# Kernel tuning notes

Measured on AMD Instinct MI355X. Metric: run time of the kernel, lower is better.

Reference implementation:

```python
import jax, jax.numpy as jnp
import numpy as np

D_MODEL = 1024
N_HEADS = 16
D_K = D_MODEL // N_HEADS
B, S = 2, 2048


def setup_inputs() -> dict:
    key = jax.random.key(0)
    ks = jax.random.split(key, 12)
    s = 1.0 / np.sqrt(D_MODEL)
    inp = {
        "query": jax.random.normal(ks[0], (B, S, D_MODEL), jnp.float32),
        "key": jax.random.normal(ks[1], (B, S, D_MODEL), jnp.float32),
        "value": jax.random.normal(ks[2], (B, S, D_MODEL), jnp.float32),
        "W_q": jax.random.uniform(ks[3], (D_MODEL, D_MODEL), jnp.float32, -s, s),
        "b_q": jnp.zeros((D_MODEL,), jnp.float32),
        "W_k": jax.random.uniform(ks[4], (D_MODEL, D_MODEL), jnp.float32, -s, s),
        "b_k": jnp.zeros((D_MODEL,), jnp.float32),
        "W_v": jax.random.uniform(ks[5], (D_MODEL, D_MODEL), jnp.float32, -s, s),
        "b_v": jnp.zeros((D_MODEL,), jnp.float32),
        "W_o": jax.random.uniform(ks[6], (D_MODEL, D_MODEL), jnp.float32, -s, s),
        "b_o": jnp.zeros((D_MODEL,), jnp.float32),
        "ln_gamma": jnp.ones((D_MODEL,), jnp.float32),
        "ln_beta": jnp.zeros((D_MODEL,), jnp.float32),
    }
    return inp


def _layer_norm(x, gamma, beta, eps=1e-5):
    mu = jnp.mean(x, axis=-1, keepdims=True)
    var = jnp.var(x, axis=-1, keepdims=True)
    return (x - mu) * jax.lax.rsqrt(var + eps) * gamma + beta


def reference(query, key, value, W_q, b_q, W_k, b_k, W_v, b_v, W_o, b_o, ln_gamma, ln_beta):
    b, s, _ = query.shape
    # projections -> [b, h, s, d_k]
    q = (query @ W_q.T + b_q).reshape(b, s, N_HEADS, D_K).transpose(0, 2, 1, 3)
    k = (key @ W_k.T + b_k).reshape(b, s, N_HEADS, D_K).transpose(0, 2, 1, 3)
    v = (value @ W_v.T + b_v).reshape(b, s, N_HEADS, D_K).transpose(0, 2, 1, 3)
    # scaled dot-product attention (no mask)
    scores = jnp.einsum('bhqd,bhkd->bhqk', q, k) / jnp.sqrt(jnp.float32(D_K))
    attn = jax.nn.softmax(scores, axis=-1)
    ctx = jnp.einsum('bhqk,bhkd->bhqd', attn, v)  # [b,h,s,d_k]
    ctx = ctx.transpose(0, 2, 1, 3).reshape(b, s, D_MODEL)
    out = ctx @ W_o.T + b_o
    # residual uses the PROJECTED query (quirk of original module); dropout=identity (eval)
    resid = q.transpose(0, 2, 1, 3).reshape(b, s, D_MODEL)
    return _layer_norm(out + resid, ln_gamma, ln_beta)
```

## Files before the change

kernel.cpp:

```cpp
#include <hip/hip_runtime.h>

#define DM 1024
#define NH 16
#define DKq 64
#define BB 2
#define SS 2048
#define MTOT 4096

typedef __attribute__((ext_vector_type(4))) float f32x4;
typedef __attribute__((ext_vector_type(16))) float f32x16;
typedef __attribute__((ext_vector_type(8))) short s16x8;
typedef __attribute__((ext_vector_type(4))) short s16x4;
typedef __attribute__((ext_vector_type(4))) unsigned short u16x4;

__device__ __forceinline__ unsigned short f2bf(float f) {
    unsigned u = __float_as_uint(f);
    u += 0x7fff + ((u >> 16) & 1);
    return (unsigned short)(u >> 16);
}

__device__ __forceinline__ float bf2f(unsigned short x) {
    return __uint_as_float((unsigned)x << 16);
}

__device__ __forceinline__ s16x8 cvt8(f32x4 a, f32x4 b) {
    s16x8 r;
    r[0] = (short)f2bf(a[0]); r[1] = (short)f2bf(a[1]);
    r[2] = (short)f2bf(a[2]); r[3] = (short)f2bf(a[3]);
    r[4] = (short)f2bf(b[0]); r[5] = (short)f2bf(b[1]);
    r[6] = (short)f2bf(b[2]); r[7] = (short)f2bf(b[3]);
    return r;
}

__device__ __forceinline__ unsigned pktr(float a, float b) {
    return (__float_as_uint(a) >> 16) | (__float_as_uint(b) & 0xFFFF0000u);
}

__device__ __forceinline__ void gload_lds16(const void* g, void* l) {
    __builtin_amdgcn_global_load_lds(
        (const __attribute__((address_space(1))) unsigned int*)g,
        (__attribute__((address_space(3))) unsigned int*)l,
        16, 0, 0);
}

__global__ __launch_bounds__(256)
void cvt_kernel(const float* __restrict__ s0, const float* __restrict__ s1,
                const float* __restrict__ s2, const float* __restrict__ s3,
                const float* __restrict__ s4, const float* __restrict__ s5,
                const float* __restrict__ s6,
                unsigned short* __restrict__ Xb, unsigned short* __restrict__ Wb)
{
    const int seg = blockIdx.y;
    const float* src;
    unsigned short* dst;
    int n;
    if (seg < 3) {
        src = (seg == 0) ? s0 : (seg == 1) ? s1 : s2;
        dst = Xb + (size_t)seg * (MTOT * DM);
        n = MTOT * DM;
    } else {
        src = (seg == 3) ? s3 : (seg == 4) ? s4 : (seg == 5) ? s5 : s6;
        dst = Wb + (size_t)(seg - 3) * (DM * DM);
        n = DM * DM;
    }
    const int stride = gridDim.x * 256;
    for (int i = blockIdx.x * 256 + threadIdx.x; i * 8 < n; i += stride) {
        f32x4 a = *(const f32x4*)(src + (size_t)i * 8);
        f32x4 b = *(const f32x4*)(src + (size_t)i * 8 + 4);
        *(s16x8*)(dst + (size_t)i * 8) = cvt8(a, b);
    }
}

__global__ __launch_bounds__(256)
void proj_kernel(const unsigned short* __restrict__ Xb,
                 const unsigned short* __restrict__ Wb,
                 const float* __restrict__ bq, const float* __restrict__ bk,
                 const float* __restrict__ bv,
                 unsigned short* __restrict__ Qh, unsigned short* __restrict__ Kh,
                 unsigned short* __restrict__ Vt)
{
    const int z = blockIdx.z;
    const unsigned short* X = Xb + (size_t)z * (MTOT * DM);
    const unsigned short* W = Wb + (size_t)z * (DM * DM);
    const float* bias = (z == 0) ? bq : (z == 1) ? bk : bv;

    const int m0 = blockIdx.y * 128;
    const int n0 = blockIdx.x * 128;
    const int tid  = threadIdx.x;
    const int lane = tid & 63;
    const int w    = tid >> 6;
    const int wm   = w >> 1, wn = w & 1;

    __shared__ __align__(16) short lA[128 * 64];
    __shared__ __align__(16) short lB[128 * 64];

    f32x4 acc[4][4];
#pragma unroll
    for (int i = 0; i < 4; i++)
#pragma unroll
        for (int j = 0; j < 4; j++) acc[i][j] = (f32x4)(0.f);

    const int lrow = lane >> 3;
    const int lcg  = (lane & 7) ^ lrow;

    for (int kt = 0; kt < 16; ++kt) {
        const int k0 = kt * 64;
#pragma unroll
        for (int p = 0; p < 4; ++p) {
            int c = w * 4 + p;
            int row = c * 8 + lrow;
            gload_lds16(X + (size_t)(m0 + row) * DM + k0 + lcg * 8,
                        (char*)lA + c * 1024);
            gload_lds16(W + (size_t)(n0 + row) * DM + k0 + lcg * 8,
                        (char*)lB + c * 1024);
        }
        __syncthreads();
#pragma unroll
        for (int kk = 0; kk < 2; ++kk) {
            s16x8 af[4], bf[4];
#pragma unroll
            for (int i = 0; i < 4; i++) {
                int row = wm * 64 + i * 16 + (lane & 15);
                int byte = (kk * 64 + 16 * (lane >> 4)) ^ ((row & 7) << 4);
                af[i] = *(const s16x8*)((const char*)lA + row * 128 + byte);
            }
#pragma unroll
            for (int i = 0; i < 4; i++) {
                int row = wn * 64 + i * 16 + (lane & 15);
                int byte = (kk * 64 + 16 * (lane >> 4)) ^ ((row & 7) << 4);
                bf[i] = *(const s16x8*)((const char*)lB + row * 128 + byte);
            }
#pragma unroll
            for (int i = 0; i < 4; i++)
#pragma unroll
                for (int j = 0; j < 4; j++)
                    acc[i][j] = __builtin_amdgcn_mfma_f32_16x16x32_bf16(
                        af[i], bf[j], acc[i][j], 0, 0, 0);
        }
        __syncthreads();
    }

#pragma unroll
    for (int i = 0; i < 4; i++) {
#pragma unroll
        for (int j = 0; j < 4; j++) {
            int rg0 = m0 + wm * 64 + i * 16 + 4 * (lane >> 4);
            int cg  = n0 + wn * 64 + j * 16 + (lane & 15);
            int b = rg0 >> 11, s0 = rg0 & 2047, h = cg >> 6, d = cg & 63;
            float bv_ = bias[cg];
            if (z == 2) {
                u16x4 st;
#pragma unroll
                for (int e = 0; e < 4; e++) st[e] = f2bf(acc[i][j][e] + bv_);
                *(u16x4*)&Vt[(((size_t)(b * NH + h)) * DKq + d) * SS + s0] = st;
            } else {
                unsigned short* P = (z == 0) ? Qh : Kh;
#pragma unroll
                for (int e = 0; e < 4; e++)
                    P[(((size_t)(b * NH + h)) * SS + s0 + e) * DKq + d] =
                        f2bf(acc[i][j][e] + bv_);
            }
        }
    }
}

__device__ __forceinline__ void attn_tile32(
    const char* __restrict__ lkc, const char* __restrict__ lvc,
    const s16x8* aq, int l31, int hi,
    f32x16& o0, f32x16& o1, float& lrun)
{
    const float K2 = 0.18033688011112042f;
    const float FS = 4.0f * K2;

    f32x16 s0 = (f32x16)(0.f), s1 = (f32x16)(0.f);
    __builtin_amdgcn_s_setprio(1);
#pragma unroll
    for (int kkd = 0; kkd < 4; kkd++) {
        {
            int row = l31;
            int byte = (32 * kkd + 16 * hi) ^ ((row & 7) << 4);
            s16x8 ak = *(const s16x8*)(lkc + row * 128 + byte);
            s0 = __builtin_amdgcn_mfma_f32_32x32x16_bf16(ak, aq[kkd], s0, 0, 0, 0);
        }
        {
            int row = 32 + l31;
            int byte = (32 * kkd + 16 * hi) ^ ((row & 7) << 4);
            s16x8 ak = *(const s16x8*)(lkc + row * 128 + byte);
            s1 = __builtin_amdgcn_mfma_f32_32x32x16_bf16(ak, aq[kkd], s1, 0, 0, 0);
        }
    }
    __builtin_amdgcn_s_setprio(0);

    float rs = 0.f;
#pragma unroll
    for (int r = 0; r < 16; r++) {
        float p0 = __builtin_amdgcn_exp2f(__builtin_fmaf(s0[r], K2, -FS));
        float p1 = __builtin_amdgcn_exp2f(__builtin_fmaf(s1[r], K2, -FS));
        s0[r] = p0; s1[r] = p1;
        rs += p0 + p1;
    }
    lrun += rs;

    __builtin_amdgcn_s_setprio(1);
#pragma unroll
    for (int jb = 0; jb < 2; jb++) {
#pragma unroll
        for (int u = 0; u < 2; u++) {
            const int t = 2 * jb + u;
            union { unsigned uu[4]; s16x8 v; } bp;
            if (jb == 0) {
                bp.uu[0] = pktr(s0[8*u+0], s0[8*u+1]);
                bp.uu[1] = pktr(s0[8*u+2], s0[8*u+3]);
                bp.uu[2] = pktr(s0[8*u+4], s0[8*u+5]);
                bp.uu[3] = pktr(s0[8*u+6], s0[8*u+7]);
            } else {
                bp.uu[0] = pktr(s1[8*u+0], s1[8*u+1]);
                bp.uu[1] = pktr(s1[8*u+2], s1[8*u+3]);
                bp.uu[2] = pktr(s1[8*u+4], s1[8*u+5]);
                bp.uu[3] = pktr(s1[8*u+6], s1[8*u+7]);
            }
            {
                int row = l31;
                int sw = (row & 7) << 4;
                union { s16x4 h2[2]; s16x8 v; } av;
                av.h2[0] = *(const s16x4*)(lvc + row * 128 + ((32*t + 8*hi) ^ sw));
                av.h2[1] = *(const s16x4*)(lvc + row * 128 + ((32*t + 16 + 8*hi) ^ sw));
                o0 = __builtin_amdgcn_mfma_f32_32x32x16_bf16(av.v, bp.v, o0, 0, 0, 0);
            }
            {
                int row = 32 + l31;
                int sw = (row & 7) << 4;
                union { s16x4 h2[2]; s16x8 v; } av;
                av.h2[0] = *(const s16x4*)(lvc + row * 128 + ((32*t + 8*hi) ^ sw));
                av.h2[1] = *(const s16x4*)(lvc + row * 128 + ((32*t + 16 + 8*hi) ^ sw));
                o1 = __builtin_amdgcn_mfma_f32_32x32x16_bf16(av.v, bp.v, o1, 0, 0, 0);
            }
        }
    }
    __builtin_amdgcn_s_setprio(0);
}

__global__ __launch_bounds__(256)
void attn_kernel(const unsigned short* __restrict__ Qh,
                 const unsigned short* __restrict__ Kh,
                 const unsigned short* __restrict__ Vt,
                 unsigned short* __restrict__ Ctx)
{
    const int bh = blockIdx.y;
    const int q0 = blockIdx.x * 128;
    const int tid = threadIdx.x, lane = tid & 63, w = tid >> 6;
    const int b = bh >> 4, h = bh & 15;
    const int l31 = lane & 31;
    const int hi  = lane >> 5;

    __shared__ __align__(16) short lKs[2][64 * 64];
    __shared__ __align__(16) short lVs[2][64 * 64];

    const size_t qk_base = (size_t)bh * SS * DKq;
    const size_t vt_base = (size_t)bh * DKq * SS;

    s16x8 aq[4];
    const int qrow = q0 + 32 * w + l31;
    {
        const unsigned short* qp = Qh + qk_base + (size_t)qrow * DKq + 8 * hi;
#pragma unroll
        for (int kkd = 0; kkd < 4; kkd++)
            aq[kkd] = *(const s16x8*)(qp + 16 * kkd);
    }

    f32x16 o0 = (f32x16)(0.f), o1 = (f32x16)(0.f);
    float lrun = 0.f;

    const int lrow = lane >> 3;
    const int lcg  = (lane & 7) ^ lrow;

#define STAGE(BUF, KV0) {                                                     \
    char* dk = (char*)lKs[BUF]; char* dv = (char*)lVs[BUF];                   \
    _Pragma("unroll")                                                         \
    for (int p = 0; p < 2; ++p) {                                             \
        int c = 2 * w + p;                                                    \
        gload_lds16(Kh + qk_base + (size_t)((KV0) + c * 8 + lrow) * DKq + lcg * 8, \
                    dk + c * 1024);                                           \
        gload_lds16(Vt + vt_base + (size_t)(c * 8 + lrow) * SS + (KV0) + lcg * 8,  \
                    dv + c * 1024);                                           \
    } }

    STAGE(0, 0);
    __syncthreads();

    for (int th = 0; th < 16; ++th) {
        const int t0 = th * 2;
        STAGE(1, (t0 + 1) * 64);
        attn_tile32((const char*)lKs[0], (const char*)lVs[0], aq, l31, hi, o0, o1, lrun);
        __syncthreads();
        if (t0 + 2 < 32) STAGE(0, (t0 + 2) * 64);
        attn_tile32((const char*)lKs[1], (const char*)lVs[1], aq, l31, hi, o0, o1, lrun);
        __syncthreads();
    }
#undef STAGE

    lrun += __shfl_xor(lrun, 32);
    const float inv = 1.0f / lrun;
    unsigned short* crow = Ctx + ((size_t)(b * SS + qrow)) * DM + h * 64;
#pragma unroll
    for (int db = 0; db < 2; db++) {
#pragma unroll
        for (int v = 0; v < 4; v++) {
            u16x4 st;
#pragma unroll
            for (int e = 0; e < 4; e++) {
                float x = (db == 0) ? o0[4 * v + e] : o1[4 * v + e];
                st[e] = f2bf(x * inv);
            }
            *(u16x4*)(crow + 32 * db + 8 * v + 4 * hi) = st;
        }
    }
}

__global__ __launch_bounds__(256)
void outproj_kernel(const unsigned short* __restrict__ Ctx,
                    const unsigned short* __restrict__ Wo,
                    const float* __restrict__ bo,
                    const unsigned short* __restrict__ Qh,
                    float* __restrict__ Out)
{
    const int m0 = blockIdx.y * 128;
    const int n0 = blockIdx.x * 128;
    const int tid = threadIdx.x, lane = tid & 63, w = tid >> 6;
    const int wm = w >> 1, wn = w & 1;

    __shared__ __align__(16) short lA[128 * 64];
    __shared__ __align__(16) short lB[128 * 64];

    f32x4 acc[4][4];
#pragma unroll
    for (int i = 0; i < 4; i++)
#pragma unroll
        for (int j = 0; j < 4; j++) acc[i][j] = (f32x4)(0.f);

    const int lrow = lane >> 3;
    const int lcg  = (lane & 7) ^ lrow;

    for (int kt = 0; kt < 16; ++kt) {
        const int k0 = kt * 64;
#pragma unroll
        for (int p = 0; p < 4; ++p) {
            int c = w * 4 + p;
            int row = c * 8 + lrow;
            gload_lds16(Ctx + (size_t)(m0 + row) * DM + k0 + lcg * 8,
                        (char*)lA + c * 1024);
            gload_lds16(Wo + (size_t)(n0 + row) * DM + k0 + lcg * 8,
                        (char*)lB + c * 1024);
        }
        __syncthreads();
#pragma unroll
        for (int kk = 0; kk < 2; ++kk) {
            s16x8 af[4], bf[4];
#pragma unroll
            for (int i = 0; i < 4; i++) {
                int row = wm * 64 + i * 16 + (lane & 15);
                int byte = (kk * 64 + 16 * (lane >> 4)) ^ ((row & 7) << 4);
                af[i] = *(const s16x8*)((const char*)lA + row * 128 + byte);
            }
#pragma unroll
            for (int i = 0; i < 4; i++) {
                int row = wn * 64 + i * 16 + (lane & 15);
                int byte = (kk * 64 + 16 * (lane >> 4)) ^ ((row & 7) << 4);
                bf[i] = *(const s16x8*)((const char*)lB + row * 128 + byte);
            }
#pragma unroll
            for (int i = 0; i < 4; i++)
#pragma unroll
                for (int j = 0; j < 4; j++)
                    acc[i][j] = __builtin_amdgcn_mfma_f32_16x16x32_bf16(
                        af[i], bf[j], acc[i][j], 0, 0, 0);
        }
        __syncthreads();
    }

#pragma unroll
    for (int i = 0; i < 4; i++) {
#pragma unroll
        for (int j = 0; j < 4; j++) {
            int rg0 = m0 + wm * 64 + i * 16 + 4 * (lane >> 4);
            int cg  = n0 + wn * 64 + j * 16 + (lane & 15);
            int b = rg0 >> 11, s0 = rg0 & 2047, h = cg >> 6, d = cg & 63;
            float bo_ = bo[cg];
#pragma unroll
            for (int e = 0; e < 4; e++) {
                float res = bf2f(Qh[(((size_t)(b * NH + h)) * SS + s0 + e) * DKq + d]);
                Out[(size_t)(rg0 + e) * DM + cg] = acc[i][j][e] + bo_ + res;
            }
        }
    }
}

__global__ __launch_bounds__(256)
void ln_kernel(float* __restrict__ Out, const float* __restrict__ gamma,
               const float* __restrict__ beta)
{
    const int row = blockIdx.x;
    float* rp = Out + (size_t)row * DM;
    const int tid = threadIdx.x;

    f32x4 x = *(const f32x4*)(rp + tid * 4);
    float s  = x[0] + x[1] + x[2] + x[3];
    float sq = x[0] * x[0] + x[1] * x[1] + x[2] * x[2] + x[3] * x[3];
#pragma unroll
    for (int off = 1; off < 64; off <<= 1) {
        s  += __shfl_xor(s, off);
        sq += __shfl_xor(sq, off);
    }
    __shared__ float ps[4], pq[4];
    const int w = tid >> 6;
    if ((tid & 63) == 0) { ps[w] = s; pq[w] = sq; }
    __syncthreads();
    float ts = ps[0] + ps[1] + ps[2] + ps[3];
    float tq = pq[0] + pq[1] + pq[2] + pq[3];
    float mu  = ts * (1.f / 1024.f);
    float var = tq * (1.f / 1024.f) - mu * mu;
    float rst = rsqrtf(var + 1e-5f);

    f32x4 g  = *(const f32x4*)(gamma + tid * 4);
    f32x4 bt = *(const f32x4*)(beta + tid * 4);
    f32x4 y;
#pragma unroll
    for (int e = 0; e < 4; e++) y[e] = (x[e] - mu) * rst * g[e] + bt[e];
    *(f32x4*)(rp + tid * 4) = y;
}

extern "C" void kernel_launch(void* const* d_in, const int* in_sizes, int n_in,
                              void* d_out, int out_size, void* d_ws, size_t ws_size,
                              hipStream_t stream)
{
    const float* query = (const float*)d_in[0];
    const float* key   = (const float*)d_in[1];
    const float* value = (const float*)d_in[2];
    const float* Wq = (const float*)d_in[3];
    const float* bq = (const float*)d_in[4];
    const float* Wk = (const float*)d_in[5];
    const float* bk = (const float*)d_in[6];
    const float* Wv = (const float*)d_in[7];
    const float* bv = (const float*)d_in[8];
    const float* Wo = (const float*)d_in[9];
    const float* bo = (const float*)d_in[10];
    const float* gamma = (const float*)d_in[11];
    const float* beta  = (const float*)d_in[12];

    char* ws = (char*)d_ws;
    unsigned short* Xb  = (unsigned short*)(ws);
    unsigned short* Wb  = (unsigned short*)(ws + (24u << 20));
    unsigned short* Qh  = (unsigned short*)(ws + (32u << 20));
    unsigned short* Kh  = (unsigned short*)(ws + (40u << 20));
    unsigned short* Vt  = (unsigned short*)(ws + (48u << 20));
    unsigned short* Ctx = (unsigned short*)(ws);
    float* Out = (float*)d_out;

    cvt_kernel<<<dim3(256, 7), 256, 0, stream>>>(query, key, value,
                                                 Wq, Wk, Wv, Wo, Xb, Wb);
    proj_kernel<<<dim3(8, 32, 3), 256, 0, stream>>>(Xb, Wb, bq, bk, bv,
                                                    Qh, Kh, Vt);
    attn_kernel<<<dim3(16, 32), 256, 0, stream>>>(Qh, Kh, Vt, Ctx);
    outproj_kernel<<<dim3(8, 32), 256, 0, stream>>>(Ctx, Wb + 3u * DM * DM, bo,
                                                    Qh, Out);
    ln_kernel<<<4096, 256, 0, stream>>>(Out, gamma, beta);
}
```

Before: 150.4 us.

## Fold softmax scale into Q, compute row sums via MFMA, permute V layout

Pre-scales Q by the log2e/sqrt(dk) factor at projection time, so the attention inner loop becomes a bare exp2 and the residual path undoes the scale with an FMA. The fixed max-shift term is dropped, which assumes scores stay small enough to avoid overflow. The per-lane row-sum accumulation is replaced by an extra MFMA against a ones vector, which moves the adds onto the matrix unit. V^T is written with permuted sequence indices so each PV A-operand becomes one 16-byte LDS read instead of two 8-byte reads, and bf16 packing now uses v_perm. The cost is one extra MFMA per PV step and an extra accumulator register block, and bf16 rounding of the pre-scaled Q adds a small precision risk.

```diff
diff --git a/kernel.cpp b/kernel.cpp
--- a/kernel.cpp
+++ b/kernel.cpp
@@ -6,6 +6,9 @@
 #define BB 2
 #define SS 2048
 #define MTOT 4096
+
+#define K2f 0.18033688011112042f
+#define IK2f 5.545177444479562f
 
 typedef __attribute__((ext_vector_type(4))) float f32x4;
 typedef __attribute__((ext_vector_type(16))) float f32x16;
@@ -32,8 +35,8 @@
     return r;
 }
 
-__device__ __forceinline__ unsigned pktr(float a, float b) {
-    return (__float_as_uint(a) >> 16) | (__float_as_uint(b) & 0xFFFF0000u);
+__device__ __forceinline__ unsigned pkp(float a, float b) {
+    return __builtin_amdgcn_perm(__float_as_uint(b), __float_as_uint(a), 0x07060302u);
 }
 
 __device__ __forceinline__ void gload_lds16(const void* g, void* l) {
@@ -149,15 +152,20 @@
             int b = rg0 >> 11, s0 = rg0 & 2047, h = cg >> 6, d = cg & 63;
             float bv_ = bias[cg];
             if (z == 2) {
+                int s0p = (s0 & ~12) | ((s0 & 4) << 1) | ((s0 & 8) >> 1);
                 u16x4 st;
 #pragma unroll
                 for (int e = 0; e < 4; e++) st[e] = f2bf(acc[i][j][e] + bv_);
-                *(u16x4*)&Vt[(((size_t)(b * NH + h)) * DKq + d) * SS + s0] = st;
+                *(u16x4*)&Vt[(((size_t)(b * NH + h)) * DKq + d) * SS + s0p] = st;
+            } else if (z == 0) {
+#pragma unroll
+                for (int e = 0; e < 4; e++)
+                    Qh[(((size_t)(b * NH + h)) * SS + s0 + e) * DKq + d] =
+                        f2bf((acc[i][j][e] + bv_) * K2f);
             } else {
-                unsigned short* P = (z == 0) ? Qh : Kh;
 #pragma unroll
                 for (int e = 0; e < 4; e++)
-                    P[(((size_t)(b * NH + h)) * SS + s0 + e) * DKq + d] =
+                    Kh[(((size_t)(b * NH + h)) * SS + s0 + e) * DKq + d] =
                         f2bf(acc[i][j][e] + bv_);
             }
         }
@@ -166,40 +174,27 @@
 
 __device__ __forceinline__ void attn_tile32(
     const char* __restrict__ lkc, const char* __restrict__ lvc,
-    const s16x8* aq, int l31, int hi,
-    f32x16& o0, f32x16& o1, float& lrun)
-{
-    const float K2 = 0.18033688011112042f;
-    const float FS = 4.0f * K2;
-
+    const s16x8* aq, s16x8 onesv, int l31, int hi,
+    f32x16& o0, f32x16& o1, f32x16& o4)
+{
     f32x16 s0 = (f32x16)(0.f), s1 = (f32x16)(0.f);
+    const int sw = (l31 & 7) << 4;
     __builtin_amdgcn_s_setprio(1);
 #pragma unroll
     for (int kkd = 0; kkd < 4; kkd++) {
-        {
-            int row = l31;
-            int byte = (32 * kkd + 16 * hi) ^ ((row & 7) << 4);
-            s16x8 ak = *(const s16x8*)(lkc + row * 128 + byte);
-            s0 = __builtin_amdgcn_mfma_f32_32x32x16_bf16(ak, aq[kkd], s0, 0, 0, 0);
-        }
-        {
-            int row = 32 + l31;
-            int byte = (32 * kkd + 16 * hi) ^ ((row & 7) << 4);
-            s16x8 ak = *(const s16x8*)(lkc + row * 128 + byte);
-            s1 = __builtin_amdgcn_mfma_f32_32x32x16_bf16(ak, aq[kkd], s1, 0, 0, 0);
-        }
+        const int byte = (32 * kkd + 16 * hi) ^ sw;
+        s16x8 ak0 = *(const s16x8*)(lkc + l31 * 128 + byte);
+        s0 = __builtin_amdgcn_mfma_f32_32x32x16_bf16(ak0, aq[kkd], s0, 0, 0, 0);
+        s16x8 ak1 = *(const s16x8*)(lkc + (32 + l31) * 128 + byte);
+        s1 = __builtin_amdgcn_mfma_f32_32x32x16_bf16(ak1, aq[kkd], s1, 0, 0, 0);
     }
     __builtin_amdgcn_s_setprio(0);
 
-    float rs = 0.f;
 #pragma unroll
     for (int r = 0; r < 16; r++) {
-        float p0 = __builtin_amdgcn_exp2f(__builtin_fmaf(s0[r], K2, -FS));
-        float p1 = __builtin_amdgcn_exp2f(__builtin_fmaf(s1[r], K2, -FS));
-        s0[r] = p0; s1[r] = p1;
-        rs += p0 + p1;
-    }
-    lrun += rs;
+        s0[r] = __builtin_amdgcn_exp2f(s0[r]);
+        s1[r] = __builtin_amdgcn_exp2f(s1[r]);
+    }
 
     __builtin_amdgcn_s_setprio(1);
 #pragma unroll
@@ -209,32 +204,22 @@
             const int t = 2 * jb + u;
             union { unsigned uu[4]; s16x8 v; } bp;
             if (jb == 0) {
-                bp.uu[0] = pktr(s0[8*u+0], s0[8*u+1]);
-                bp.uu[1] = pktr(s0[8*u+2], s0[8*u+3]);
-                bp.uu[2] = pktr(s0[8*u+4], s0[8*u+5]);
-                bp.uu[3] = pktr(s0[8*u+6], s0[8*u+7]);
+                bp.uu[0] = pkp(s0[8*u+0], s0[8*u+1]);
+                bp.uu[1] = pkp(s0[8*u+2], s0[8*u+3]);
+                bp.uu[2] = pkp(s0[8*u+4], s0[8*u+5]);
+                bp.uu[3] = pkp(s0[8*u+6], s0[8*u+7]);
             } else {
-                bp.uu[0] = pktr(s1[8*u+0], s1[8*u+1]);
-                bp.uu[1] = pktr(s1[8*u+2], s1[8*u+3]);
-                bp.uu[2] = pktr(s1[8*u+4], s1[8*u+5]);
-                bp.uu[3] = pktr(s1[8*u+6], s1[8*u+7]);
-            }
-            {
-                int row = l31;
-                int sw = (row & 7) << 4;
-                union { s16x4 h2[2]; s16x8 v; } av;
-                av.h2[0] = *(const s16x4*)(lvc + row * 128 + ((32*t + 8*hi) ^ sw));
-                av.h2[1] = *(const s16x4*)(lvc + row * 128 + ((32*t + 16 + 8*hi) ^ sw));
-                o0 = __builtin_amdgcn_mfma_f32_32x32x16_bf16(av.v, bp.v, o0, 0, 0, 0);
-            }
-            {
-                int row = 32 + l31;
-                int sw = (row & 7) << 4;
-                union { s16x4 h2[2]; s16x8 v; } av;
-                av.h2[0] = *(const s16x4*)(lvc + row * 128 + ((32*t + 8*hi) ^ sw));
-                av.h2[1] = *(const s16x4*)(lvc + row * 128 + ((32*t + 16 + 8*hi) ^ sw));
-                o1 = __builtin_amdgcn_mfma_f32_32x32x16_bf16(av.v, bp.v, o1, 0, 0, 0);
-            }
+                bp.uu[0] = pkp(s1[8*u+0], s1[8*u+1]);
+                bp.uu[1] = pkp(s1[8*u+2], s1[8*u+3]);
+                bp.uu[2] = pkp(s1[8*u+4], s1[8*u+5]);
+                bp.uu[3] = pkp(s1[8*u+6], s1[8*u+7]);
+            }
+            const int vbyte = (32 * t + 16 * hi) ^ sw;
+            s16x8 av0 = *(const s16x8*)(lvc + l31 * 128 + vbyte);
+            o0 = __builtin_amdgcn_mfma_f32_32x32x16_bf16(av0, bp.v, o0, 0, 0, 0);
+            s16x8 av1 = *(const s16x8*)(lvc + (32 + l31) * 128 + vbyte);
+            o1 = __builtin_amdgcn_mfma_f32_32x32x16_bf16(av1, bp.v, o1, 0, 0, 0);
+            o4 = __builtin_amdgcn_mfma_f32_32x32x16_bf16(onesv, bp.v, o4, 0, 0, 0);
         }
     }
     __builtin_amdgcn_s_setprio(0);
@@ -268,8 +253,11 @@
             aq[kkd] = *(const s16x8*)(qp + 16 * kkd);
     }
 
-    f32x16 o0 = (f32x16)(0.f), o1 = (f32x16)(0.f);
-    float lrun = 0.f;
+    s16x8 onesv;
+#pragma unroll
+    for (int i = 0; i < 8; i++) onesv[i] = (short)0x3F80;
+
+    f32x16 o0 = (f32x16)(0.f), o1 = (f32x16)(0.f), o4 = (f32x16)(0.f);
 
     const int lrow = lane >> 3;
     const int lcg  = (lane & 7) ^ lrow;
@@ -291,16 +279,15 @@
     for (int th = 0; th < 16; ++th) {
         const int t0 = th * 2;
         STAGE(1, (t0 + 1) * 64);
-        attn_tile32((const char*)lKs[0], (const char*)lVs[0], aq, l31, hi, o0, o1, lrun);
+        attn_tile32((const char*)lKs[0], (const char*)lVs[0], aq, onesv, l31, hi, o0, o1, o4);
         __syncthreads();
         if (t0 + 2 < 32) STAGE(0, (t0 + 2) * 64);
-        attn_tile32((const char*)lKs[1], (const char*)lVs[1], aq, l31, hi, o0, o1, lrun);
+        attn_tile32((const char*)lKs[1], (const char*)lVs[1], aq, onesv, l31, hi, o0, o1, o4);
         __syncthreads();
     }
 #undef STAGE
 
-    lrun += __shfl_xor(lrun, 32);
-    const float inv = 1.0f / lrun;
+    const float inv = 1.0f / o4[0];
     unsigned short* crow = Ctx + ((size_t)(b * SS + qrow)) * DM + h * 64;
 #pragma unroll
     for (int db = 0; db < 2; db++) {
@@ -389,7 +376,8 @@
 #pragma unroll
             for (int e = 0; e < 4; e++) {
                 float res = bf2f(Qh[(((size_t)(b * NH + h)) * SS + s0 + e) * DKq + d]);
-                Out[(size_t)(rg0 + e) * DM + cg] = acc[i][j][e] + bo_ + res;
+                Out[(size_t)(rg0 + e) * DM + cg] =
+                    __builtin_fmaf(res, IK2f, acc[i][j][e] + bo_);
             }
         }
     }
```

Result: faster. 143.8 us (-4.4%).
